# Performance work log

Measured on AMD Instinct MI355X. Metric: run time of the kernel, lower is better.

Reference implementation:

```python
import jax, jax.numpy as jnp
import numpy as np

H, DK, D, DFF = 8, 64, 512, 512
B, S = 4, 1024
SCALE = 1.0 / np.sqrt(DK)


def _ln(x, g, b, eps=1e-5):
    m = jnp.mean(x, axis=-1, keepdims=True)
    v = jnp.mean((x - m) ** 2, axis=-1, keepdims=True)
    return (x - m) / jnp.sqrt(v + eps) * g + b


def _heads(x, w, b):
    bs, s, _ = x.shape
    return (x @ w + b).reshape(bs, s, H, DK).transpose(0, 2, 1, 3)  # [B,H,S,DK]


def _encoder_layer(x, qw, qb, kw, kb, vw, vb, ow, ob, g1, b1, w1, c1, w2, c2, g2, b2):
    # standard post-LN transformer encoder layer (sub_attention.Encoder(1))
    q = _heads(x, qw, qb)
    k = _heads(x, kw, kb)
    v = _heads(x, vw, vb)
    attn = jax.nn.softmax(jnp.einsum('bhqd,bhkd->bhqk', q, k) * SCALE, axis=-1)
    ctx = jnp.einsum('bhqk,bhkd->bhqd', attn, v).transpose(0, 2, 1, 3).reshape(x.shape[0], -1, H * DK)
    h = _ln(ctx @ ow + ob + x, g1, b1)
    f = jax.nn.relu(h @ w1 + c1) @ w2 + c2
    return _ln(f + h, g2, b2)


def setup_inputs() -> dict:
    key = jax.random.key(0)
    ks = iter(jax.random.split(key, 80))

    def nrm(*shape):
        return jax.random.normal(next(ks), shape, jnp.float32) * 0.02

    inp = {'audio_feat': jax.random.normal(next(ks), (B, S, D), jnp.float32),
           'video_feat': jax.random.normal(next(ks), (B, S, D), jnp.float32)}
    for p in ['aq', 'ak', 'av', 'vq', 'vk', 'vv', 'out']:
        inp[p + '_w'] = nrm(D, D)
        inp[p + '_b'] = jnp.zeros((D,), jnp.float32)
    inp['ln_g'] = jnp.ones((D,), jnp.float32)
    inp['ln_b'] = jnp.zeros((D,), jnp.float32)
    for pfx in ['asa_', 'vsa_']:
        for wn in ['qw', 'kw', 'vw', 'ow']:
            inp[pfx + wn] = nrm(D, D)
        for bn in ['qb', 'kb', 'vb', 'ob']:
            inp[pfx + bn] = jnp.zeros((D,), jnp.float32)
        inp[pfx + 'w1'] = nrm(D, DFF)
        inp[pfx + 'c1'] = jnp.zeros((DFF,), jnp.float32)
        inp[pfx + 'w2'] = nrm(DFF, D)
        inp[pfx + 'c2'] = jnp.zeros((D,), jnp.float32)
        inp[pfx + 'g1'] = jnp.ones((D,), jnp.float32)
        inp[pfx + 'b1'] = jnp.zeros((D,), jnp.float32)
        inp[pfx + 'g2'] = jnp.ones((D,), jnp.float32)
        inp[pfx + 'b2'] = jnp.zeros((D,), jnp.float32)
    return inp


def reference(audio_feat, video_feat, aq_w, aq_b, ak_w, ak_b, av_w, av_b, vq_w, vq_b, vk_w, vk_b, vv_w, vv_b, out_w, out_b, ln_g, ln_b, asa_qw, asa_qb, asa_kw, asa_kb, asa_vw, asa_vb, asa_ow, asa_ob, asa_g1, asa_b1, asa_w1, asa_c1, asa_w2, asa_c2, asa_g2, asa_b2, vsa_qw, vsa_qb, vsa_kw, vsa_kb, vsa_vw, vsa_vb, vsa_ow, vsa_ob, vsa_g1, vsa_b1, vsa_w1, vsa_c1, vsa_w2, vsa_c2, vsa_g2, vsa_b2):
    audio_self = _encoder_layer(audio_feat, asa_qw, asa_qb, asa_kw, asa_kb, asa_vw, asa_vb, asa_ow, asa_ob, asa_g1, asa_b1, asa_w1, asa_c1, asa_w2, asa_c2, asa_g2, asa_b2)
    video_self = _encoder_layer(video_feat, vsa_qw, vsa_qb, vsa_kw, vsa_kb, vsa_vw, vsa_vb, vsa_ow, vsa_ob, vsa_g1, vsa_b1, vsa_w1, vsa_c1, vsa_w2, vsa_c2, vsa_g2, vsa_b2)
    qa = _heads(audio_feat, aq_w, aq_b)
    ka = _heads(audio_feat, ak_w, ak_b)
    va = _heads(audio_feat, av_w, av_b)
    qv = _heads(video_feat, vq_w, vq_b)
    kv = _heads(video_feat, vk_w, vk_b)
    vvh = _heads(video_feat, vv_w, vv_b)
    attn_a = jax.nn.softmax(jnp.einsum('bhqd,bhkd->bhqk', qa, ka) * SCALE, axis=-1)
    attn_v = jax.nn.softmax(jnp.einsum('bhqd,bhkd->bhqk', qv, kv) * SCALE, axis=-1)
    attn = attn_a * attn_v  # dual-softmax elementwise combine
    ctx = jnp.einsum('bhqk,bhkd->bhqd', attn, va) * jnp.einsum('bhqk,bhkd->bhqd', attn, vvh)
    ctx = ctx.transpose(0, 2, 1, 3).reshape(audio_feat.shape[0], -1, H * DK)
    context = ctx @ out_w + out_b
    return _ln(audio_feat + context + audio_self + video_self, ln_g, ln_b)
```

## Files before the change

kernel.cpp:

```cpp
#include <hip/hip_runtime.h>
#include <cstddef>
#include <cstdint>


typedef __attribute__((ext_vector_type(8))) short s8v;
typedef __attribute__((ext_vector_type(4))) short s4v;
typedef __attribute__((ext_vector_type(4))) float f4v;

#define QSC 0.1803368801111444f
#define EXP2(x) __builtin_amdgcn_exp2f(x)
#define WAITV(N) asm volatile("s_waitcnt vmcnt(" #N ")" ::: "memory")
#define BAR() __builtin_amdgcn_s_barrier()
#define PRIO(n) __builtin_amdgcn_s_setprio(n)

static __device__ __forceinline__ short f2bf(float f){
  unsigned int u = __builtin_bit_cast(unsigned int, f);
  u += 0x7fffu + ((u >> 16) & 1u);
  return (short)(u >> 16);
}
static __device__ __forceinline__ float bf2f(short s){
  unsigned int u = ((unsigned int)(unsigned short)s) << 16;
  return __builtin_bit_cast(float, u);
}
static __device__ __forceinline__ void gload16(const void* g, void* l){
  __builtin_amdgcn_global_load_lds(
      (const __attribute__((address_space(1))) unsigned int*)g,
      (__attribute__((address_space(3))) unsigned int*)l, 16, 0, 0);
}
#define MFMA16(a,b,c) __builtin_amdgcn_mfma_f32_16x16x32_bf16(a,b,c,0,0,0)

struct Ptr19 { const float* p[19]; };

__global__ __launch_bounds__(256) void prep(const float* __restrict__ a,
                                            const float* __restrict__ v,
                                            short* __restrict__ oa,
                                            short* __restrict__ ov,
                                            Ptr19 ws, short* __restrict__ wp){
  const int b = blockIdx.x, tid = threadIdx.x;
  if (b < 2048){
    const float* src = (b >= 1024) ? v : a;
    short* dst = (b >= 1024) ? ov : oa;
    const int i = ((b & 1023) * 256 + tid) * 8;
    float4 x = *reinterpret_cast<const float4*>(src + i);
    float4 y = *reinterpret_cast<const float4*>(src + i + 4);
    s8v o;
    o[0]=f2bf(x.x); o[1]=f2bf(x.y); o[2]=f2bf(x.z); o[3]=f2bf(x.w);
    o[4]=f2bf(y.x); o[5]=f2bf(y.y); o[6]=f2bf(y.z); o[7]=f2bf(y.w);
    *reinterpret_cast<s8v*>(dst + i) = o;
  } else {
    const int pb = b - 2048;
    const int mat = pb >> 7;
    const float* W = ws.p[mat];
    const int f = (pb & 127) * 256 + tid;
    const int nblk = f >> 10, kg = (f >> 4) & 63, nl = f & 15;
    const int n = nblk * 16 + nl, k = kg * 8;
    s8v o;
#pragma unroll
    for (int e = 0; e < 8; ++e) o[e] = f2bf(W[(size_t)(k + e) * 512 + n]);
    *reinterpret_cast<s8v*>(wp + (size_t)mat * 262144 + (size_t)f * 8) = o;
  }
}

struct GemmJobs { const short* A[12]; const short* W[12]; const float* bias[12];
                  short* C[12]; int mode[12]; };

__global__ __launch_bounds__(256, 2) void gemm_wide(GemmJobs J){
  int i = (blockIdx.z * 32 + blockIdx.y) * 2 + blockIdx.x;
  const int c = (64 * gridDim.z) >> 3;
  i = (i & 7) * c + (i >> 3);
  const int z = i >> 6, rem = i & 63;
  const int by = rem >> 1, bx = rem & 1;

  const short* __restrict__ A = J.A[z];
  const short* __restrict__ Wp = J.W[z];
  const float* __restrict__ bias = J.bias[z];
  short* __restrict__ C = J.C[z];
  const int md = J.mode[z];
  __shared__ short smem[36864];
  const int tid = threadIdx.x, lane = tid & 63, w = tid >> 6;
  const int wm = w >> 1, wn = w & 1;
  const int m0 = by * 128, n0 = bx * 256;
  const int lh = lane >> 4, ll = lane & 15;
  f4v acc[4][8] = {};

  auto stage = [&](int kt, int buf){
    const int k0 = kt * 32;
    short* As = smem + buf * 4096;
    short* Bs = smem + 12288 + buf * 8192;
#pragma unroll
    for (int p = 0; p < 2; ++p){
      const int f = tid + 256 * p;
      const int blk = f >> 6, kg = (f >> 4) & 3, il = f & 15;
      gload16(A + (size_t)(m0 + blk * 16 + il) * 512 + k0 + kg * 8, As + f * 8);
    }
#pragma unroll
    for (int p = 0; p < 4; ++p){
      const int f = tid + 256 * p;
      const int cblk = f >> 6, kg = (f >> 4) & 3, il = f & 15;
      gload16(Wp + ((size_t)(((n0 >> 4) + cblk) * 64 + (k0 >> 3) + kg) * 16 + il) * 8,
              Bs + f * 8);
    }
  };

  stage(0, 0);
  stage(1, 1);
#pragma unroll 1
  for (int kt = 0; kt < 16; ++kt){
    if (kt < 15) { WAITV(6); } else { WAITV(0); }
    BAR();
    if (kt < 14) stage(kt + 2, (kt + 2) % 3);
    const int cur = kt % 3;
    const short* As = smem + cur * 4096;
    const short* Bs = smem + 12288 + cur * 8192;
    s8v a[4], b[8];
#pragma unroll
    for (int q = 0; q < 4; ++q)
      a[q] = *reinterpret_cast<const s8v*>(&As[(((wm*4+q)*4 + lh)*16 + ll) * 8]);
#pragma unroll
    for (int j = 0; j < 8; ++j)
      b[j] = *reinterpret_cast<const s8v*>(&Bs[(((wn*8+j)*4 + lh)*16 + ll) * 8]);
    PRIO(1);
#pragma unroll
    for (int q = 0; q < 4; ++q)
#pragma unroll
      for (int j = 0; j < 8; ++j)
        acc[q][j] = MFMA16(a[q], b[j], acc[q][j]);
    PRIO(0);
  }
  BAR();

  if (md == 2){
#pragma unroll
    for (int j = 0; j < 8; ++j){
      const int col = n0 + wn * 128 + j * 16 + ll;
      const float bv = bias[col];
      const int hh = col >> 6, dl = col & 63, dblk = dl >> 4, il = dl & 15;
#pragma unroll
      for (int q = 0; q < 4; ++q){
        const int rowb = m0 + wm * 64 + q * 16 + lh * 4;
        const int bb = rowb >> 10, srow = rowb & 1023;
        const size_t off = ((size_t)((bb*8 + hh)*16 + (srow >> 6))) * 4096
                         + (size_t)(((dblk << 7) + (((srow >> 3) & 7) << 4) + il) * 8 + (srow & 7));
        s4v o4;
#pragma unroll
        for (int r = 0; r < 4; ++r) o4[r] = f2bf(acc[q][j][r] + bv);
        *reinterpret_cast<s4v*>(&C[off]) = o4;
      }
    }
  } else {
    short* epi = smem + w * 8192;
    const float sc = (md == 1) ? QSC : 1.0f;
#pragma unroll
    for (int j = 0; j < 8; ++j){
      const float bv = bias[n0 + wn * 128 + j * 16 + ll];
#pragma unroll
      for (int q = 0; q < 4; ++q)
#pragma unroll
        for (int r = 0; r < 4; ++r)
          epi[(q*16 + lh*4 + r)*128 + j*16 + ll] = f2bf((acc[q][j][r] + bv) * sc);
    }
#pragma unroll
    for (int i2 = 0; i2 < 16; ++i2){
      const int row = i2 * 4 + (lane >> 4);
      s8v vr = *reinterpret_cast<const s8v*>(&epi[row*128 + (lane & 15)*8]);
      *reinterpret_cast<s8v*>(&C[(size_t)(m0 + wm*64 + row)*512 + n0 + wn*128 + (lane&15)*8]) = vr;
    }
  }
}

template<bool RELU>
__global__ __launch_bounds__(256) void gemm_n64(GemmJobs J){
  int i = (blockIdx.z * 32 + blockIdx.y) * 8 + blockIdx.x;
  const int c = (256 * gridDim.z) >> 3;
  i = (i & 7) * c + (i >> 3);
  const int z = i >> 8, rem = i & 255;
  const int by = rem >> 3, bx = rem & 7;

  const short* __restrict__ A = J.A[z];
  const short* __restrict__ Wp = J.W[z];
  const float* __restrict__ bias = J.bias[z];
  short* __restrict__ C = J.C[z];
  __shared__ short As[3][4096], Bs[3][2048];
  const int tid = threadIdx.x, lane = tid & 63, w = tid >> 6;
  const int wm = w >> 1, wn = w & 1;
  const int m0 = by * 128, n0 = bx * 64;
  const int lh = lane >> 4, ll = lane & 15;
  f4v acc[4][2] = {};

  auto stage = [&](int kt, int buf){
    const int k0 = kt * 32;
#pragma unroll
    for (int p = 0; p < 2; ++p){
      const int f = tid + 256 * p;
      const int blk = f >> 6, kg = (f >> 4) & 3, il = f & 15;
      gload16(A + (size_t)(m0 + blk * 16 + il) * 512 + k0 + kg * 8, &As[buf][f * 8]);
    }
    {
      const int f = tid;
      const int blk = f >> 6, kg = (f >> 4) & 3, il = f & 15;
      gload16(Wp + ((size_t)(((n0 >> 4) + blk) * 64 + (k0 >> 3) + kg) * 16 + il) * 8,
              &Bs[buf][f * 8]);
    }
  };

  stage(0, 0);
  stage(1, 1);
#pragma unroll 1
  for (int kt = 0; kt < 16; ++kt){
    if (kt < 15) { WAITV(3); } else { WAITV(0); }
    BAR();
    if (kt < 14) stage(kt + 2, (kt + 2) % 3);
    const int cur = kt % 3;
    s8v a[4], b[2];
#pragma unroll
    for (int q = 0; q < 4; ++q)
      a[q] = *reinterpret_cast<const s8v*>(&As[cur][(((wm*4+q)*4 + lh)*16 + ll) * 8]);
#pragma unroll
    for (int j = 0; j < 2; ++j)
      b[j] = *reinterpret_cast<const s8v*>(&Bs[cur][(((wn*2+j)*4 + lh)*16 + ll) * 8]);
    PRIO(1);
#pragma unroll
    for (int q = 0; q < 4; ++q)
#pragma unroll
      for (int j = 0; j < 2; ++j)
        acc[q][j] = MFMA16(a[q], b[j], acc[q][j]);
    PRIO(0);
  }
  BAR();

  short* epi = &As[0][0] + w * 2048;
#pragma unroll
  for (int j = 0; j < 2; ++j){
    const float bv = bias[n0 + wn * 32 + j * 16 + ll];
#pragma unroll
    for (int q = 0; q < 4; ++q)
#pragma unroll
      for (int r = 0; r < 4; ++r){
        float v = acc[q][j][r] + bv;
        if (RELU) v = fmaxf(v, 0.f);
        epi[(q*16 + lh*4 + r)*32 + j*16 + ll] = f2bf(v);
      }
  }
#pragma unroll
  for (int i2 = 0; i2 < 4; ++i2){
    const int row = i2 * 16 + (lane >> 2);
    s8v vr = *reinterpret_cast<const s8v*>(&epi[row*32 + (lane & 3)*8]);
    *reinterpret_cast<s8v*>(&C[(size_t)(m0 + wm*64 + row)*512 + n0 + wn*32 + (lane&3)*8]) = vr;
  }
}

struct AttnJob { const short* Q; const short* K; const short* Vp; short* O; };

__global__ __launch_bounds__(512) void attn_enc(AttnJob j0, AttnJob j1){
  const AttnJob jb = blockIdx.z ? j1 : j0;
  __shared__ short KT[2][4096], VT[2][4096];
  __shared__ short PL[8][1024];
  const int tid = threadIdx.x, lane = tid & 63, w = tid >> 6;
  int bi = blockIdx.y * 8 + blockIdx.x;
  bi = (bi & 7) * 32 + (bi >> 3);
  const int qt = bi & 7, bh = bi >> 3;
  const int b = bh >> 3, h = bh & 7;
  const int q0 = qt * 128;
  const size_t base = (size_t)b * 1024 * 512 + (size_t)h * 64;
  const int lh = lane >> 4, ll = lane & 15;
  short* PLw = PL[w];

  s8v qf[2];
#pragma unroll
  for (int df = 0; df < 2; ++df)
    qf[df] = *reinterpret_cast<const s8v*>(jb.Q + base + (size_t)(q0 + w*16 + ll)*512 + lh*8 + df*32);

  const int sblk = tid >> 7, sg8 = (tid >> 4) & 7, sil = tid & 15;
  auto stage = [&](int it, int buf){
    gload16(jb.K + base + (size_t)(it*64 + sblk*16 + sil)*512 + sg8*8, &KT[buf][tid*8]);
    gload16(jb.Vp + ((size_t)bh*16 + it)*4096 + (size_t)tid*8, &VT[buf][tid*8]);
  };

  f4v o[4] = {};
  float zacc = 0.f;
  const int pwo = ((lh >> 1) * 16 + ll) * 8 + (lh & 1) * 4;
  const int pro = ((lh) * 16 + ll) * 8;

  stage(0, 0);
#pragma unroll 1
  for (int it = 0; it < 16; ++it){
    if (it < 15) { stage(it + 1, (it + 1) & 1); WAITV(2); }
    else         { WAITV(0); }
    BAR();
    const int cur = it & 1;

    f4v s[4] = {};
    PRIO(1);
#pragma unroll
    for (int fn = 0; fn < 4; ++fn)
#pragma unroll
      for (int df = 0; df < 2; ++df){
        s8v kf = *reinterpret_cast<const s8v*>(&KT[cur][((fn*8 + lh + df*4)*16 + ll) * 8]);
        s[fn] = MFMA16(kf, qf[df], s[fn]);
      }
    PRIO(0);

#pragma unroll
    for (int fn = 0; fn < 4; ++fn){
      s4v p4;
#pragma unroll
      for (int r = 0; r < 4; ++r){
        const float p = EXP2(s[fn][r]);
        zacc += p;
        p4[r] = f2bf(p);
      }
      *reinterpret_cast<s4v*>(&PLw[fn*256 + pwo]) = p4;
    }
    s8v pa[2];
#pragma unroll
    for (int kf2 = 0; kf2 < 2; ++kf2)
      pa[kf2] = *reinterpret_cast<const s8v*>(&PLw[kf2*512 + pro]);
    PRIO(1);
#pragma unroll
    for (int fd = 0; fd < 4; ++fd)
#pragma unroll
      for (int kf2 = 0; kf2 < 2; ++kf2){
        s8v vf = *reinterpret_cast<const s8v*>(&VT[cur][((fd*8 + lh + kf2*4)*16 + ll) * 8]);
        o[fd] = MFMA16(vf, pa[kf2], o[fd]);
      }
    PRIO(0);
    BAR();
  }

  float Z = zacc;
  Z += __shfl_xor(Z, 16); Z += __shfl_xor(Z, 32);
  const float rz = 1.f / Z;
#pragma unroll
  for (int fd = 0; fd < 4; ++fd){
    s4v o4;
#pragma unroll
    for (int r = 0; r < 4; ++r) o4[r] = f2bf(o[fd][r] * rz);
    *reinterpret_cast<s4v*>(&jb.O[base + (size_t)(q0 + w*16 + ll)*512 + fd*16 + lh*4]) = o4;
  }
}

__global__ __launch_bounds__(512) void attn_dual(const short* __restrict__ Qa, const short* __restrict__ Ka,
                                                 const short* __restrict__ Vap, const short* __restrict__ Qv,
                                                 const short* __restrict__ Kv, const short* __restrict__ Vvp,
                                                 short* __restrict__ O){
  __shared__ short smem[36864];
  const int tid = threadIdx.x, lane = tid & 63, w = tid >> 6;
  const int qw = w & 3, kh = w >> 2;
  int bi = blockIdx.y * 16 + blockIdx.x;
  bi = (bi & 7) * 64 + (bi >> 3);
  const int qt = bi & 15, bh = bi >> 4;
  const int b = bh >> 3, h = bh & 7;
  const int q0 = qt * 64;
  const size_t base = (size_t)b * 1024 * 512 + (size_t)h * 64;
  const int lh = lane >> 4, ll = lane & 15;
  short* PLw = smem + 32768 + w * 512;

  s8v qfa[2], qfv[2];
#pragma unroll
  for (int df = 0; df < 2; ++df){
    const size_t ro = base + (size_t)(q0 + qw*16 + ll)*512 + lh*8 + df*32;
    qfa[df] = *reinterpret_cast<const s8v*>(Qa + ro);
    qfv[df] = *reinterpret_cast<const s8v*>(Qv + ro);
  }

  const int hh = tid >> 8;
  const int u = tid & 255;
  const int kblk = u >> 7, kg8 = (u >> 4) & 7, kil = u & 15;
  const int vdb = u >> 6, vk4 = (u >> 4) & 3,  vil = u & 15;

  auto stage = [&](int it, int buf){
    const int dso = hh * 4096 + buf * 2048 + u * 8;
    const size_t krow = base + (size_t)(hh*512 + it*32 + kblk*16 + kil)*512 + kg8*8;
    gload16(Ka + krow, smem + dso);
    gload16(Kv + krow, smem + 8192 + dso);
    const int kt16 = hh*8 + (it >> 1);
    const int kgrp = (it & 1)*4 + vk4;
    const size_t voff = ((size_t)bh*16 + kt16)*4096 + (size_t)((vdb*8 + kgrp)*16 + vil)*8;
    gload16(Vap + voff, smem + 16384 + dso);
    gload16(Vvp + voff, smem + 24576 + dso);
  };

  f4v oa[4] = {}, ov[4] = {};
  float za = 0.f, zv = 0.f;
  const int pwo = ((lh >> 1) * 16 + ll) * 8 + (lh & 1) * 4;
  const int pro = (lh * 16 + ll) * 8;

  stage(0, 0);
#pragma unroll 1
  for (int it = 0; it < 16; ++it){
    if (it < 15) { stage(it + 1, (it + 1) & 1); WAITV(4); }
    else         { WAITV(0); }
    BAR();
    const int cur = it & 1;
    const int to = kh * 4096 + cur * 2048;
    const short* pKa = smem + to;
    const short* pKv = smem + 8192 + to;
    const short* pVa = smem + 16384 + to;
    const short* pVv = smem + 24576 + to;

    f4v sa[2] = {}, sv[2] = {};
    PRIO(1);
#pragma unroll
    for (int fn = 0; fn < 2; ++fn)
#pragma unroll
      for (int df = 0; df < 2; ++df){
        const int boff = (fn*128 + (lh + df*4)*16 + ll) * 8;
        s8v ka = *reinterpret_cast<const s8v*>(&pKa[boff]);
        s8v kv = *reinterpret_cast<const s8v*>(&pKv[boff]);
        sa[fn] = MFMA16(ka, qfa[df], sa[fn]);
        sv[fn] = MFMA16(kv, qfv[df], sv[fn]);
      }
    PRIO(0);

#pragma unroll
    for (int fn = 0; fn < 2; ++fn){
      s4v p4;
#pragma unroll
      for (int r = 0; r < 4; ++r){
        const float ea = EXP2(sa[fn][r]);
        const float ev = EXP2(sv[fn][r]);
        za += ea; zv += ev;
        p4[r] = f2bf(ea * ev);
      }
      *reinterpret_cast<s4v*>(&PLw[fn*256 + pwo]) = p4;
    }
    s8v pa = *reinterpret_cast<const s8v*>(&PLw[pro]);
    PRIO(1);
#pragma unroll
    for (int fd = 0; fd < 4; ++fd){
      const int voff2 = (fd*64 + lh*16 + ll) * 8;
      s8v va = *reinterpret_cast<const s8v*>(&pVa[voff2]);
      s8v vv = *reinterpret_cast<const s8v*>(&pVv[voff2]);
      oa[fd] = MFMA16(va, pa, oa[fd]);
      ov[fd] = MFMA16(vv, pa, ov[fd]);
    }
    PRIO(0);
    BAR();
  }

  float* cb = (float*)smem;
  const int idx = qw * 64 + lane;
  if (kh == 1){
#pragma unroll
    for (int fd = 0; fd < 4; ++fd)
#pragma unroll
      for (int r = 0; r < 4; ++r){
        cb[(fd*4 + r)*256 + idx] = oa[fd][r];
        cb[(16 + fd*4 + r)*256 + idx] = ov[fd][r];
      }
    cb[32*256 + idx] = za;
    cb[33*256 + idx] = zv;
  }
  BAR();
  if (kh == 0){
#pragma unroll
    for (int fd = 0; fd < 4; ++fd)
#pragma unroll
      for (int r = 0; r < 4; ++r){
        oa[fd][r] += cb[(fd*4 + r)*256 + idx];
        ov[fd][r] += cb[(16 + fd*4 + r)*256 + idx];
      }
    float Za = za + cb[32*256 + idx];
    float Zv = zv + cb[33*256 + idx];
    Za += __shfl_xor(Za, 16); Za += __shfl_xor(Za, 32);
    Zv += __shfl_xor(Zv, 16); Zv += __shfl_xor(Zv, 32);
    const float rz = 1.f / (Za * Zv);
#pragma unroll
    for (int fd = 0; fd < 4; ++fd){
      s4v o4;
#pragma unroll
      for (int r = 0; r < 4; ++r){
        const float v = (oa[fd][r] * rz) * (ov[fd][r] * rz);
        o4[r] = f2bf(v);
      }
      *reinterpret_cast<s4v*>(&O[base + (size_t)(q0 + qw*16 + ll)*512 + fd*16 + lh*4]) = o4;
    }
  }
}

struct LnJob { const short* xb0; const short* xb1; const short* xb2;
               const float* xf; const float* g; const float* bb; void* out; };

template<int NBF, bool ADDF32, bool OUTF32>
__global__ __launch_bounds__(256) void ln_fused(LnJob j0, LnJob j1){
  const LnJob j = blockIdx.y ? j1 : j0;
  const int row = blockIdx.x, t = threadIdx.x;
  const size_t base = (size_t)row * 512;
  float x[2];
#pragma unroll
  for (int u = 0; u < 2; ++u){
    const int c = t + u * 256;
    float v = bf2f(j.xb0[base + c]);
    if (NBF > 1) v += bf2f(j.xb1[base + c]);
    if (NBF > 2) v += bf2f(j.xb2[base + c]);
    if (ADDF32) v += j.xf[base + c];
    x[u] = v;
  }
  float s = x[0] + x[1], ss = x[0]*x[0] + x[1]*x[1];
#pragma unroll
  for (int o = 32; o; o >>= 1){ s += __shfl_xor(s, o); ss += __shfl_xor(ss, o); }
  __shared__ float rb[8];
  const int wv = t >> 6;
  if ((t & 63) == 0){ rb[wv] = s; rb[wv + 4] = ss; }
  __syncthreads();
  s  = rb[0] + rb[1] + rb[2] + rb[3];
  ss = rb[4] + rb[5] + rb[6] + rb[7];
  const float m = s * (1.f / 512.f);
  const float var = ss * (1.f / 512.f) - m * m;
  const float rstd = rsqrtf(var + 1e-5f);
#pragma unroll
  for (int u = 0; u < 2; ++u){
    const int c = t + u * 256;
    const float v = (x[u] - m) * rstd * j.g[c] + j.bb[c];
    if (OUTF32) ((float*)j.out)[base + c] = v;
    else        ((short*)j.out)[base + c] = f2bf(v);
  }
}

__global__ __launch_bounds__(256) void ln_final(const short* __restrict__ fa, const short* __restrict__ ha,
                                                const short* __restrict__ fv, const short* __restrict__ hv,
                                                const short* __restrict__ ctx, const float* __restrict__ audio,
                                                const float* __restrict__ g2a, const float* __restrict__ b2a,
                                                const float* __restrict__ g2v, const float* __restrict__ b2v,
                                                const float* __restrict__ gf, const float* __restrict__ bf,
                                                float* __restrict__ out){
  const int row = blockIdx.x, t = threadIdx.x;
  const size_t base = (size_t)row * 512;
  __shared__ float rb[24];
  const int wv = t >> 6;

  auto reduce2 = [&](float a, float b, int p){
    float s = a + b, ss = a*a + b*b;
#pragma unroll
    for (int o = 32; o; o >>= 1){ s += __shfl_xor(s, o); ss += __shfl_xor(ss, o); }
    if ((t & 63) == 0){ rb[p*8 + wv] = s; rb[p*8 + 4 + wv] = ss; }
  };
  auto stats = [&](int p, float& m, float& rstd){
    const float s  = rb[p*8+0] + rb[p*8+1] + rb[p*8+2] + rb[p*8+3];
    const float ss = rb[p*8+4] + rb[p*8+5] + rb[p*8+6] + rb[p*8+7];
    m = s * (1.f / 512.f);
    rstd = rsqrtf(ss * (1.f / 512.f) - m * m + 1e-5f);
  };

  float xa[2], xv[2];
#pragma unroll
  for (int u = 0; u < 2; ++u){
    const int c = t + u * 256;
    xa[u] = bf2f(fa[base + c]) + bf2f(ha[base + c]);
    xv[u] = bf2f(fv[base + c]) + bf2f(hv[base + c]);
  }
  reduce2(xa[0], xa[1], 0);
  reduce2(xv[0], xv[1], 1);
  __syncthreads();
  float ma, ra, mv, rv;
  stats(0, ma, ra);
  stats(1, mv, rv);

  float xf[2];
#pragma unroll
  for (int u = 0; u < 2; ++u){
    const int c = t + u * 256;
    const float sa = (xa[u] - ma) * ra * g2a[c] + b2a[c];
    const float sv = (xv[u] - mv) * rv * g2v[c] + b2v[c];
    xf[u] = audio[base + c] + bf2f(ctx[base + c]) + sa + sv;
  }
  reduce2(xf[0], xf[1], 2);
  __syncthreads();
  float mf, rf;
  stats(2, mf, rf);
#pragma unroll
  for (int u = 0; u < 2; ++u){
    const int c = t + u * 256;
    out[base + c] = (xf[u] - mf) * rf * gf[c] + bf[c];
  }
}

extern "C" void kernel_launch(void* const* d_in, const int* in_sizes, int n_in,
                              void* d_out, int out_size, void* d_ws, size_t ws_size,
                              hipStream_t stream) {
  const float* audio = (const float*)d_in[0];
  const float* video = (const float*)d_in[1];
  auto F = [&](int i){ return (const float*)d_in[i]; };

  short* ws16 = (short*)d_ws;
  const size_t SL = 2097152;
  auto S = [&](int i){ return ws16 + (size_t)i * SL; };
  short* Wp = S(12);
  auto WP = [&](int i){ return (const short*)(Wp + (size_t)i * 262144); };
  short* Kcv = (short*)d_out;
  short* Vcv = (short*)d_out + SL;

  Ptr19 pw;
  const int widx[19] = {18,19,20,21,26,28, 34,35,36,37,42,44, 2,4,6,8,10,12, 14};
  for (int i = 0; i < 19; ++i) pw.p[i] = F(widx[i]);
  prep<<<4480, 256, 0, stream>>>(audio, video, S(10), S(11), pw, Wp);

  GemmJobs g1{};
  const short* g1A[12] = {S(10),S(10),S(10), S(11),S(11),S(11), S(10),S(10),S(10), S(11),S(11),S(11)};
  const short* g1W[12] = {WP(0),WP(1),WP(2), WP(6),WP(7),WP(8), WP(12),WP(13),WP(14), WP(15),WP(16),WP(17)};
  const float* g1B[12] = {F(22),F(23),F(24), F(38),F(39),F(40), F(3),F(5),F(7), F(9),F(11),F(13)};
  short*       g1C[12] = {S(0),S(1),S(2), S(3),S(4),S(5), S(6),S(7),S(8), S(9),Kcv,Vcv};
  const int    g1M[12] = {1,0,2, 1,0,2, 1,0,2, 1,0,2};
  for (int i = 0; i < 12; ++i){ g1.A[i]=g1A[i]; g1.W[i]=g1W[i]; g1.bias[i]=g1B[i]; g1.C[i]=g1C[i]; g1.mode[i]=g1M[i]; }
  gemm_wide<<<dim3(2,32,12), 256, 0, stream>>>(g1);

  attn_enc<<<dim3(8,32,2), 512, 0, stream>>>(AttnJob{S(0),S(1),S(2),S(10)},
                                             AttnJob{S(3),S(4),S(5),S(11)});

  attn_dual<<<dim3(16,32), 512, 0, stream>>>(S(6),S(7),S(8), S(9),Kcv,Vcv, S(0));

  GemmJobs g39{};
  g39.A[0]=S(10); g39.W[0]=WP(3);  g39.bias[0]=F(25); g39.C[0]=S(1); g39.mode[0]=0;
  g39.A[1]=S(11); g39.W[1]=WP(9);  g39.bias[1]=F(41); g39.C[1]=S(2); g39.mode[1]=0;
  g39.A[2]=S(0);  g39.W[2]=WP(18); g39.bias[2]=F(15); g39.C[2]=S(3); g39.mode[2]=0;
  gemm_n64<false><<<dim3(8,32,3), 256, 0, stream>>>(g39);

  ln_fused<1,true,false><<<dim3(4096,2), 256, 0, stream>>>(
      LnJob{S(1),nullptr,nullptr, audio, F(30),F(31), S(4)},
      LnJob{S(2),nullptr,nullptr, video, F(46),F(47), S(5)});

  GemmJobs g5{};
  g5.A[0]=S(4); g5.W[0]=WP(4);  g5.bias[0]=F(27); g5.C[0]=S(6); g5.mode[0]=0;
  g5.A[1]=S(5); g5.W[1]=WP(10); g5.bias[1]=F(43); g5.C[1]=S(7); g5.mode[1]=0;
  gemm_n64<true><<<dim3(8,32,2), 256, 0, stream>>>(g5);

  GemmJobs g6{};
  g6.A[0]=S(6); g6.W[0]=WP(5);  g6.bias[0]=F(29); g6.C[0]=S(8); g6.mode[0]=0;
  g6.A[1]=S(7); g6.W[1]=WP(11); g6.bias[1]=F(45); g6.C[1]=S(9); g6.mode[1]=0;
  gemm_n64<false><<<dim3(8,32,2), 256, 0, stream>>>(g6);

  ln_final<<<4096, 256, 0, stream>>>(S(8),S(4), S(9),S(5), S(3), audio,
                                     F(32),F(33), F(48),F(49), F(16),F(17),
                                     (float*)d_out);
}
```

Baseline: 173.7 us.

## Split encoder attention keys across two wave halves with smaller query tiles

```diff
diff --git a/kernel.cpp b/kernel.cpp
--- a/kernel.cpp
+++ b/kernel.cpp
@@ -251,35 +251,43 @@
 
 struct AttnJob { const short* Q; const short* K; const short* Vp; short* O; };
 
-__global__ __launch_bounds__(512) void attn_enc(AttnJob j0, AttnJob j1){
+__global__ __launch_bounds__(512, 8) void attn_enc(AttnJob j0, AttnJob j1){
   const AttnJob jb = blockIdx.z ? j1 : j0;
-  __shared__ short KT[2][4096], VT[2][4096];
-  __shared__ short PL[8][1024];
+  __shared__ short smem[20480];
   const int tid = threadIdx.x, lane = tid & 63, w = tid >> 6;
-  int bi = blockIdx.y * 8 + blockIdx.x;
-  bi = (bi & 7) * 32 + (bi >> 3);
-  const int qt = bi & 7, bh = bi >> 3;
+  const int qw = w & 3, kh = w >> 2;
+  int bi = blockIdx.y * 16 + blockIdx.x;
+  bi = (bi & 7) * 64 + (bi >> 3);
+  const int qt = bi & 15, bh = bi >> 4;
   const int b = bh >> 3, h = bh & 7;
-  const int q0 = qt * 128;
+  const int q0 = qt * 64;
   const size_t base = (size_t)b * 1024 * 512 + (size_t)h * 64;
   const int lh = lane >> 4, ll = lane & 15;
-  short* PLw = PL[w];
+  short* PLw = smem + 16384 + w * 512;
 
   s8v qf[2];
 #pragma unroll
   for (int df = 0; df < 2; ++df)
-    qf[df] = *reinterpret_cast<const s8v*>(jb.Q + base + (size_t)(q0 + w*16 + ll)*512 + lh*8 + df*32);
-
-  const int sblk = tid >> 7, sg8 = (tid >> 4) & 7, sil = tid & 15;
+    qf[df] = *reinterpret_cast<const s8v*>(jb.Q + base + (size_t)(q0 + qw*16 + ll)*512 + lh*8 + df*32);
+
+  const int hh = tid >> 8;
+  const int u = tid & 255;
+  const int kblk = u >> 7, kg8 = (u >> 4) & 7, kil = u & 15;
+  const int vdb = u >> 6, vk4 = (u >> 4) & 3,  vil = u & 15;
+
   auto stage = [&](int it, int buf){
-    gload16(jb.K + base + (size_t)(it*64 + sblk*16 + sil)*512 + sg8*8, &KT[buf][tid*8]);
-    gload16(jb.Vp + ((size_t)bh*16 + it)*4096 + (size_t)tid*8, &VT[buf][tid*8]);
+    const int dso = hh * 4096 + buf * 2048 + u * 8;
+    gload16(jb.K + base + (size_t)(hh*512 + it*32 + kblk*16 + kil)*512 + kg8*8, smem + dso);
+    const int kt16 = hh*8 + (it >> 1);
+    const int kgrp = (it & 1)*4 + vk4;
+    gload16(jb.Vp + ((size_t)bh*16 + kt16)*4096 + (size_t)((vdb*8 + kgrp)*16 + vil)*8,
+            smem + 8192 + dso);
   };
 
   f4v o[4] = {};
   float zacc = 0.f;
   const int pwo = ((lh >> 1) * 16 + ll) * 8 + (lh & 1) * 4;
-  const int pro = ((lh) * 16 + ll) * 8;
+  const int pro = (lh * 16 + ll) * 8;
 
   stage(0, 0);
 #pragma unroll 1
@@ -287,21 +295,23 @@
     if (it < 15) { stage(it + 1, (it + 1) & 1); WAITV(2); }
     else         { WAITV(0); }
     BAR();
-    const int cur = it & 1;
-
-    f4v s[4] = {};
+    const int to = kh * 4096 + (it & 1) * 2048;
+    const short* pK = smem + to;
+    const short* pV = smem + 8192 + to;
+
+    f4v s[2] = {};
     PRIO(1);
 #pragma unroll
-    for (int fn = 0; fn < 4; ++fn)
+    for (int fn = 0; fn < 2; ++fn)
 #pragma unroll
       for (int df = 0; df < 2; ++df){
-        s8v kf = *reinterpret_cast<const s8v*>(&KT[cur][((fn*8 + lh + df*4)*16 + ll) * 8]);
+        s8v kf = *reinterpret_cast<const s8v*>(&pK[(fn*128 + (lh + df*4)*16 + ll) * 8]);
         s[fn] = MFMA16(kf, qf[df], s[fn]);
       }
     PRIO(0);
 
 #pragma unroll
-    for (int fn = 0; fn < 4; ++fn){
+    for (int fn = 0; fn < 2; ++fn){
       s4v p4;
 #pragma unroll
       for (int r = 0; r < 4; ++r){
@@ -311,31 +321,42 @@
       }
       *reinterpret_cast<s4v*>(&PLw[fn*256 + pwo]) = p4;
     }
-    s8v pa[2];
-#pragma unroll
-    for (int kf2 = 0; kf2 < 2; ++kf2)
-      pa[kf2] = *reinterpret_cast<const s8v*>(&PLw[kf2*512 + pro]);
+    s8v pa = *reinterpret_cast<const s8v*>(&PLw[pro]);
     PRIO(1);
 #pragma unroll
-    for (int fd = 0; fd < 4; ++fd)
-#pragma unroll
-      for (int kf2 = 0; kf2 < 2; ++kf2){
-        s8v vf = *reinterpret_cast<const s8v*>(&VT[cur][((fd*8 + lh + kf2*4)*16 + ll) * 8]);
-        o[fd] = MFMA16(vf, pa[kf2], o[fd]);
-      }
+    for (int fd = 0; fd < 4; ++fd){
+      s8v vf = *reinterpret_cast<const s8v*>(&pV[(fd*64 + lh*16 + ll) * 8]);
+      o[fd] = MFMA16(vf, pa, o[fd]);
+    }
     PRIO(0);
     BAR();
   }
 
-  float Z = zacc;
-  Z += __shfl_xor(Z, 16); Z += __shfl_xor(Z, 32);
-  const float rz = 1.f / Z;
-#pragma unroll
-  for (int fd = 0; fd < 4; ++fd){
-    s4v o4;
-#pragma unroll
-    for (int r = 0; r < 4; ++r) o4[r] = f2bf(o[fd][r] * rz);
-    *reinterpret_cast<s4v*>(&jb.O[base + (size_t)(q0 + w*16 + ll)*512 + fd*16 + lh*4]) = o4;
+  float* cb = (float*)smem;
+  const int idx = qw * 64 + lane;
+  if (kh == 1){
+#pragma unroll
+    for (int fd = 0; fd < 4; ++fd)
+#pragma unroll
+      for (int r = 0; r < 4; ++r) cb[(fd*4 + r)*256 + idx] = o[fd][r];
+    cb[16*256 + idx] = zacc;
+  }
+  BAR();
+  if (kh == 0){
+#pragma unroll
+    for (int fd = 0; fd < 4; ++fd)
+#pragma unroll
+      for (int r = 0; r < 4; ++r) o[fd][r] += cb[(fd*4 + r)*256 + idx];
+    float Z = zacc + cb[16*256 + idx];
+    Z += __shfl_xor(Z, 16); Z += __shfl_xor(Z, 32);
+    const float rz = 1.f / Z;
+#pragma unroll
+    for (int fd = 0; fd < 4; ++fd){
+      s4v o4;
+#pragma unroll
+      for (int r = 0; r < 4; ++r) o4[r] = f2bf(o[fd][r] * rz);
+      *reinterpret_cast<s4v*>(&jb.O[base + (size_t)(q0 + qw*16 + ll)*512 + fd*16 + lh*4]) = o4;
+    }
   }
 }
 
@@ -604,8 +625,8 @@
   for (int i = 0; i < 12; ++i){ g1.A[i]=g1A[i]; g1.W[i]=g1W[i]; g1.bias[i]=g1B[i]; g1.C[i]=g1C[i]; g1.mode[i]=g1M[i]; }
   gemm_wide<<<dim3(2,32,12), 256, 0, stream>>>(g1);
 
-  attn_enc<<<dim3(8,32,2), 512, 0, stream>>>(AttnJob{S(0),S(1),S(2),S(10)},
-                                             AttnJob{S(3),S(4),S(5),S(11)});
+  attn_enc<<<dim3(16,32,2), 512, 0, stream>>>(AttnJob{S(0),S(1),S(2),S(10)},
+                                              AttnJob{S(3),S(4),S(5),S(11)});
 
   attn_dual<<<dim3(16,32), 512, 0, stream>>>(S(6),S(7),S(8), S(9),Kcv,Vcv, S(0));
 
```

After: 176.5 us. About the same (+1.6%).
